# Performance work log

Measured on AMD Instinct MI355X. Metric: run time of the kernel, lower is better.

The kernel has to match this reference:

```python
import jax, jax.numpy as jnp
import numpy as np

B, P, D = 64, 196, 768
HP = WP = 14
N_CLASSES = 200
C = N_CLASSES + 1
K_PROTO = 5
GAMMA = 0.999
TEMP = 0.2
EPS_SK = 0.05
SK_ITERS = 3


def l2norm(x, axis=-1, eps=1e-12):
    n = jnp.linalg.norm(x, axis=axis, keepdims=True)
    return x / jnp.maximum(n, eps)


def _safe_div(a, b):
    return a / jnp.where(b > 0, b, 1.0)


def masked_sinkhorn(L_cnk, mask):
    """Vectorized per-class Sinkhorn-Knopp over masked patch groups.
    L_cnk: [C, N, K] logits; mask: [C, N] bool (patch n belongs to class c).
    Returns Q: [C, K, N] (columns of each present class sum to 1)."""
    m = mask[:, None, :].astype(L_cnk.dtype)  # [C,1,N]
    Q = jnp.exp(jnp.transpose(L_cnk, (0, 2, 1)) / EPS_SK) * m  # [C,K,N]
    Q = _safe_div(Q, Q.sum(axis=(1, 2), keepdims=True))
    Nc = mask.sum(axis=1).astype(Q.dtype)[:, None, None]  # per-class patch count
    Nc_safe = jnp.where(Nc > 0, Nc, 1.0)
    for _ in range(SK_ITERS):
        Q = _safe_div(Q, Q.sum(axis=2, keepdims=True)) / K_PROTO  # row (prototype) norm
        Q = _safe_div(Q, Q.sum(axis=1, keepdims=True)) / Nc_safe  # col (patch) norm
    Q = Q * Nc  # undo final /Nc -> each patch column sums to 1
    return Q


def setup_inputs() -> dict:
    key = jax.random.key(0)
    k1, k2, k3, k4, k5 = jax.random.split(key, 5)
    patch_tokens = jax.random.normal(k1, (B, P, D), dtype=jnp.float32)
    raw_patch_tokens = jax.random.normal(k2, (B, P, D), dtype=jnp.float32)
    prototypes = 0.02 * jax.random.normal(k3, (C, K_PROTO, D), dtype=jnp.float32)
    sa_weights = jnp.full((N_CLASSES, K_PROTO), 0.5, dtype=jnp.float32)
    pseudo_patch_labels = jax.random.randint(k5, (B, HP, WP), 0, C, dtype=jnp.int32)
    return {
        "patch_tokens": patch_tokens,
        "raw_patch_tokens": raw_patch_tokens,
        "prototypes": prototypes,
        "sa_weights": sa_weights,
        "pseudo_patch_labels": pseudo_patch_labels,
    }


def reference(patch_tokens, raw_patch_tokens, prototypes, sa_weights, pseudo_patch_labels):
    # --- patch-prototype cosine similarity ---
    pt = l2norm(patch_tokens)                       # [B,P,D]
    proto_n = l2norm(prototypes)                    # [C,K,D]
    logits = jnp.einsum('bpd,ckd->bpck', pt, proto_n)  # [B,P,C,K]
    image_logits = logits.max(axis=1)               # [B,C,K]
    # --- ScoreAggregation classifier ---
    sw = jax.nn.softmax(sa_weights, axis=-1) * K_PROTO  # [n_classes,K]
    class_logits = (image_logits[:, :-1, :] * sw).sum(-1) / TEMP  # [B,n_classes]
    # --- online clustering (detached in original) ---
    rpt = l2norm(raw_patch_tokens)
    patches_flat = rpt.reshape(-1, D)               # [N,D], N=B*P
    labels_flat = pseudo_patch_labels.reshape(-1)   # [N]
    N = labels_flat.shape[0]
    L_nck = logits.reshape(N, C, K_PROTO)
    L_cnk = jnp.transpose(L_nck, (1, 0, 2))         # [C,N,K]
    mask = labels_flat[None, :] == jnp.arange(C)[:, None]  # [C,N]
    Q = masked_sinkhorn(L_cnk, mask)                # [C,K,N]
    # grouped GEMM: P_c_new = Q_c @ I_c for every class at once
    P_new_c = jnp.einsum('ckn,nd->ckd', Q, patches_flat)  # [C,K,D]
    present = mask.any(axis=1)[:, None, None]
    P_new = jnp.where(present,
                      GAMMA * prototypes + (1.0 - GAMMA) * P_new_c,
                      prototypes)
    # part assignment: argmax_k Q[label_n, k, n] + label_n * K
    Q_nck = jnp.transpose(Q, (2, 0, 1))             # [N,C,K]
    Q_at = Q_nck[jnp.arange(N), labels_flat]        # [N,K]
    assign = jnp.argmax(Q_at, axis=-1).astype(jnp.int32) + labels_flat * K_PROTO
    part_assignment_maps = assign.reshape(B, HP * WP)
    return (logits, image_logits, class_logits, part_assignment_maps, P_new)
```

## Files before the change

kernel.cpp:

```cpp
#include <hip/hip_runtime.h>
#include <math.h>

#define B_ 64
#define P_ 196
#define D_ 768
#define C_ 201
#define K_ 5
#define N_ (B_*P_)
#define CK_ (C_*K_)
#define NPAD 1024
#define NCLS 200
#define GAMMA_ 0.999f
#define INV_TEMP 5.0f
#define INV_EPS 20.0f
#define CAP2 256
#define EPAD 8
#define ROWS_TOT (2*N_ + NPAD)

typedef short s16x8 __attribute__((ext_vector_type(8)));
typedef float f32x4 __attribute__((ext_vector_type(4)));
typedef unsigned short u16x4 __attribute__((ext_vector_type(4)));

typedef __attribute__((address_space(3))) void lds_void;
typedef __attribute__((address_space(1))) const void g_void;
#define GLD16(gp, lp) __builtin_amdgcn_global_load_lds((g_void*)(gp), (lds_void*)(lp), 16, 0, 0)

__device__ __forceinline__ unsigned short f2bf(float f) {
    unsigned int u = __float_as_uint(f);
    unsigned int r = (u + 0x7FFFu + ((u >> 16) & 1u)) >> 16;
    return (unsigned short)r;
}

__global__ __launch_bounds__(256) void norm_all_kernel(
        const float* __restrict__ patch, const float* __restrict__ rawp,
        const float* __restrict__ proto, float* __restrict__ invR,
        unsigned short* __restrict__ Abf, unsigned short* __restrict__ Bbf,
        int* __restrict__ cnt) {
    if (blockIdx.x == 0 && threadIdx.x < C_) cnt[threadIdx.x] = 0;
    int gw = blockIdx.x * 4 + (threadIdx.x >> 6);
    int lane = threadIdx.x & 63;
    const float* src; unsigned short* dst; int realR; int r; bool wantInv = false;
    if (gw < N_) { r = gw; src = patch; dst = Abf; realR = N_; }
    else if (gw < 2 * N_) { r = gw - N_; src = rawp; dst = nullptr; realR = N_; wantInv = true; }
    else { r = gw - 2 * N_; src = proto; dst = Bbf; realR = CK_; }
    unsigned short* brow = dst ? dst + (size_t)r * D_ : nullptr;
    if (r >= realR) {
        u16x4 z = (u16x4)0;
        *(u16x4*)(brow + lane * 4)       = z;
        *(u16x4*)(brow + lane * 4 + 256) = z;
        *(u16x4*)(brow + lane * 4 + 512) = z;
        return;
    }
    const float4* row4 = (const float4*)(src + (size_t)r * D_);
    float4 v0 = row4[lane], v1 = row4[lane + 64], v2 = row4[lane + 128];
    float s = v0.x*v0.x + v0.y*v0.y + v0.z*v0.z + v0.w*v0.w
            + v1.x*v1.x + v1.y*v1.y + v1.z*v1.z + v1.w*v1.w
            + v2.x*v2.x + v2.y*v2.y + v2.z*v2.z + v2.w*v2.w;
#pragma unroll
    for (int o = 1; o < 64; o <<= 1) s += __shfl_xor(s, o, 64);
    float sc = 1.f / fmaxf(sqrtf(s), 1e-12f);
    if (brow) {
        u16x4 p0 = { f2bf(v0.x*sc), f2bf(v0.y*sc), f2bf(v0.z*sc), f2bf(v0.w*sc) };
        u16x4 p1 = { f2bf(v1.x*sc), f2bf(v1.y*sc), f2bf(v1.z*sc), f2bf(v1.w*sc) };
        u16x4 p2 = { f2bf(v2.x*sc), f2bf(v2.y*sc), f2bf(v2.z*sc), f2bf(v2.w*sc) };
        *(u16x4*)(brow + lane * 4)       = p0;
        *(u16x4*)(brow + lane * 4 + 256) = p1;
        *(u16x4*)(brow + lane * 4 + 512) = p2;
    } else if (wantInv && lane == 0) invR[r] = sc;
}

#define BM2 256
#define BN2 256
#define BK2 64
#define KT (D_/BK2)
#define MT2 (N_/BM2)
__global__ __launch_bounds__(512, 2) void gemm_mfma_kernel(
    const unsigned short* __restrict__ Ab, const unsigned short* __restrict__ Bb,
    float* __restrict__ Cc,
    float* __restrict__ part) {
    __shared__ union {
        struct { short A[2][BM2 * BK2]; short B[2][BN2 * BK2]; } g;
        float mw[2][3][BN2];
    } u;
    int tid = threadIdx.x;
    int wid = tid >> 6;
    int lane = tid & 63;
    int wr = wid >> 2, wc = wid & 3;
    int mrow = lane & 15, q = lane >> 4;
    int slot0 = q ^ (mrow & 7);

    int orig = blockIdx.x;
    int xcd = orig & 7, idx = orig >> 3;
    int wg = (xcd < 4 ? xcd * 25 : 100 + (xcd - 4) * 24) + idx;
    int mtile = wg >> 2, ntile = wg & 3;
    int mBase = mtile * BM2;
    int nBase = ntile * BN2;

    f32x4 acc[8][4];
#pragma unroll
    for (int i = 0; i < 8; ++i)
#pragma unroll
        for (int j = 0; j < 4; ++j) acc[i][j] = (f32x4)(0.f);

    const unsigned short* gA[4];
    const unsigned short* gB[4];
    int lof[4];
#pragma unroll
    for (int s = 0; s < 4; ++s) {
        int c = tid + 512 * s;
        int row = c >> 3, ch = c & 7;
        int chx = ch ^ (row & 7);
        gA[s] = Ab + (size_t)(mBase + row) * D_ + chx * 8;
        gB[s] = Bb + (size_t)(nBase + row) * D_ + chx * 8;
        lof[s] = c * 8;
    }
    auto stage = [&](int buf, int t) {
#pragma unroll
        for (int s = 0; s < 4; ++s) GLD16(gA[s] + t * BK2, &u.g.A[buf][lof[s]]);
#pragma unroll
        for (int s = 0; s < 4; ++s) GLD16(gB[s] + t * BK2, &u.g.B[buf][lof[s]]);
    };

    stage(0, 0);
    stage(1, 1);

    for (int t = 0; t < KT; ++t) {
        int cb = t & 1;
        if (t + 1 < KT) asm volatile("s_waitcnt vmcnt(8)" ::: "memory");
        else            asm volatile("s_waitcnt vmcnt(0)" ::: "memory");
        __builtin_amdgcn_s_barrier();
        __builtin_amdgcn_sched_barrier(0);
        const short* Ac = u.g.A[cb];
        const short* Bc = u.g.B[cb];
        s16x8 a[8][2], b01[2][2], b23[2][2];
#pragma unroll
        for (int mf = 0; mf < 8; ++mf) {
            int row = wr * 128 + mf * 16 + mrow;
            a[mf][0] = *(const s16x8*)&Ac[row * 64 + slot0 * 8];
            a[mf][1] = *(const s16x8*)&Ac[row * 64 + (slot0 ^ 4) * 8];
        }
#pragma unroll
        for (int nf = 0; nf < 2; ++nf) {
            int row = wc * 64 + nf * 16 + mrow;
            b01[nf][0] = *(const s16x8*)&Bc[row * 64 + slot0 * 8];
            b01[nf][1] = *(const s16x8*)&Bc[row * 64 + (slot0 ^ 4) * 8];
        }
#pragma unroll
        for (int nf = 0; nf < 2; ++nf) {
            int row = wc * 64 + (nf + 2) * 16 + mrow;
            b23[nf][0] = *(const s16x8*)&Bc[row * 64 + slot0 * 8];
            b23[nf][1] = *(const s16x8*)&Bc[row * 64 + (slot0 ^ 4) * 8];
        }
        __builtin_amdgcn_s_setprio(1);
#pragma unroll
        for (int mf = 0; mf < 8; ++mf)
#pragma unroll
            for (int nf = 0; nf < 2; ++nf) {
                acc[mf][nf] = __builtin_amdgcn_mfma_f32_16x16x32_bf16(
                    a[mf][0], b01[nf][0], acc[mf][nf], 0, 0, 0);
                acc[mf][nf] = __builtin_amdgcn_mfma_f32_16x16x32_bf16(
                    a[mf][1], b01[nf][1], acc[mf][nf], 0, 0, 0);
            }
        __builtin_amdgcn_s_setprio(0);
        asm volatile("s_waitcnt lgkmcnt(0)" ::: "memory");
        __builtin_amdgcn_s_barrier();
        __builtin_amdgcn_sched_barrier(0);
        if (t + 2 < KT) stage(cb, t + 2);
        __builtin_amdgcn_s_setprio(1);
#pragma unroll
        for (int mf = 0; mf < 8; ++mf)
#pragma unroll
            for (int nf = 0; nf < 2; ++nf) {
                acc[mf][nf + 2] = __builtin_amdgcn_mfma_f32_16x16x32_bf16(
                    a[mf][0], b23[nf][0], acc[mf][nf + 2], 0, 0, 0);
                acc[mf][nf + 2] = __builtin_amdgcn_mfma_f32_16x16x32_bf16(
                    a[mf][1], b23[nf][1], acc[mf][nf + 2], 0, 0, 0);
            }
        __builtin_amdgcn_s_setprio(0);
    }

#pragma unroll
    for (int m = 0; m < 8; ++m) {
        int gm = mBase + wr * 128 + m * 16 + q * 4;
#pragma unroll
        for (int j = 0; j < 4; ++j) {
            int gn = nBase + wc * 64 + j * 16 + mrow;
            if (gn < CK_) {
                Cc[(size_t)(gm + 0) * CK_ + gn] = acc[m][j][0];
                Cc[(size_t)(gm + 1) * CK_ + gn] = acc[m][j][1];
                Cc[(size_t)(gm + 2) * CK_ + gn] = acc[m][j][2];
                Cc[(size_t)(gm + 3) * CK_ + gn] = acc[m][j][3];
            }
        }
    }

    int imgA = mBase / 196;
    int rs1 = 196 * (imgA + 1) - mBase;
    int rs2 = rs1 + 196;
#pragma unroll
    for (int j = 0; j < 4; ++j) {
        float m0 = -INFINITY, m1 = -INFINITY, m2 = -INFINITY;
#pragma unroll
        for (int m = 0; m < 8; ++m) {
            int lr = wr * 128 + m * 16 + q * 4;
#pragma unroll
            for (int r = 0; r < 4; ++r) {
                float v = acc[m][j][r];
                int row = lr + r;
                if (row >= rs2) m2 = fmaxf(m2, v);
                else if (row >= rs1) m1 = fmaxf(m1, v);
                else m0 = fmaxf(m0, v);
            }
        }
        m0 = fmaxf(m0, __shfl_xor(m0, 16)); m0 = fmaxf(m0, __shfl_xor(m0, 32));
        m1 = fmaxf(m1, __shfl_xor(m1, 16)); m1 = fmaxf(m1, __shfl_xor(m1, 32));
        m2 = fmaxf(m2, __shfl_xor(m2, 16)); m2 = fmaxf(m2, __shfl_xor(m2, 32));
        if (lane < 16) {
            int col = wc * 64 + j * 16 + lane;
            u.mw[wr][0][col] = m0;
            u.mw[wr][1][col] = m1;
            u.mw[wr][2][col] = m2;
        }
    }
    __syncthreads();
    if (tid < BN2) {
#pragma unroll
        for (int s = 0; s < 3; ++s) {
            float vmax = fmaxf(u.mw[0][s][tid], u.mw[1][s][tid]);
            part[(size_t)(mtile * 3 + s) * 1024 + nBase + tid] = vmax;
        }
    }
}

__global__ __launch_bounds__(256) void post_kernel(
        const float* __restrict__ part, const float* __restrict__ saw,
        float* __restrict__ img, float* __restrict__ cls,
        const float* __restrict__ L, const int* __restrict__ labels,
        int* __restrict__ cnt, int* __restrict__ idxList, float* __restrict__ EList) {
    __shared__ float simg[CK_];
    if (blockIdx.x < B_) {
        int b = blockIdx.x;
        int t0 = (196 * b) >> 8;
        int t1 = (196 * b + 195) >> 8;
        for (int n = threadIdx.x; n < CK_; n += 256) {
            float m = -INFINITY;
            for (int t = t0; t <= t1; ++t) {
                int iA = (t << 8) / 196;
                int s = b - iA;
                m = fmaxf(m, part[(size_t)(t * 3 + s) * 1024 + n]);
            }
            img[b * CK_ + n] = m;
            simg[n] = m;
        }
        __syncthreads();
        int c = threadIdx.x;
        if (c < NCLS) {
            float w[K_];
            float mx = -INFINITY;
#pragma unroll
            for (int k = 0; k < K_; ++k) { w[k] = saw[c * K_ + k]; mx = fmaxf(mx, w[k]); }
            float ssum = 0.f;
#pragma unroll
            for (int k = 0; k < K_; ++k) { w[k] = expf(w[k] - mx); ssum += w[k]; }
            float acc = 0.f;
#pragma unroll
            for (int k = 0; k < K_; ++k)
                acc += simg[c * K_ + k] * (w[k] / ssum * (float)K_);
            cls[b * NCLS + c] = acc * INV_TEMP;
        }
    } else {
        int n = (blockIdx.x - B_) * 256 + threadIdx.x;
        if (n >= N_) return;
        int c = labels[n];
        int slot = atomicAdd(&cnt[c], 1);
        if (slot < CAP2) {
            idxList[c * CAP2 + slot] = n;
            const float* lp = L + (size_t)n * CK_ + c * K_;
            float e0 = expf(lp[0] * INV_EPS), e1 = expf(lp[1] * INV_EPS);
            float e2 = expf(lp[2] * INV_EPS), e3 = expf(lp[3] * INV_EPS);
            float e4 = expf(lp[4] * INV_EPS);
            float* ep = EList + ((size_t)c * CAP2 + slot) * EPAD;
            float4 v4 = { e0, e1, e2, e3 };
            *(float4*)ep = v4;
            ep[4] = e4;
        }
    }
}

#define NJ (CAP2/64)
__global__ __launch_bounds__(768) void sinkema_kernel(
    const int* __restrict__ cnt, const int* __restrict__ idxList,
    const float* __restrict__ EList, const float* __restrict__ invR,
    const float* __restrict__ rawP, const float* __restrict__ proto,
    float* __restrict__ outAssign, float* __restrict__ outProto) {
    int c = blockIdx.x;
    int tid = threadIdx.x;
    int Nc = cnt[c]; if (Nc > CAP2) Nc = CAP2;
    size_t protoOff = (size_t)c * K_ * D_;
    if (Nc == 0) {
        for (int i = tid; i < K_ * D_; i += 768)
            outProto[protoOff + i] = proto[protoOff + i];
        return;
    }
    __shared__ float s_w[K_][CAP2];
    __shared__ int s_idx[CAP2];
    for (int i = tid; i < CAP2; i += 768)
        s_idx[i] = (i < Nc) ? idxList[c * CAP2 + i] : 0;
    __syncthreads();

    if (tid < 64) {
        int lane = tid;
        float e[NJ][K_];
        float cn[NJ];
#pragma unroll
        for (int j = 0; j < NJ; ++j) {
            int n = j * 64 + lane;
            bool v = n < Nc;
            cn[j] = v ? 1.f : 0.f;
            const float* ep = EList + ((size_t)c * CAP2 + n) * EPAD;
            float4 v4 = v ? *(const float4*)ep : make_float4(0.f, 0.f, 0.f, 0.f);
            e[j][0] = v4.x; e[j][1] = v4.y; e[j][2] = v4.z; e[j][3] = v4.w;
            e[j][4] = v ? ep[4] : 0.f;
        }
        float r[K_];
        for (int it = 0; it < 3; ++it) {
#pragma unroll
            for (int k = 0; k < K_; ++k) {
                float s = 0.f;
#pragma unroll
                for (int j = 0; j < NJ; ++j) s += e[j][k] * cn[j];
                for (int o = 32; o > 0; o >>= 1) s += __shfl_xor(s, o, 64);
                r[k] = 1.f / ((float)K_ * s);
            }
#pragma unroll
            for (int j = 0; j < NJ; ++j) {
                float t = 0.f;
#pragma unroll
                for (int k = 0; k < K_; ++k) t += e[j][k] * r[k];
                cn[j] = (j * 64 + lane < Nc) ? 1.f / ((float)Nc * t) : 0.f;
            }
        }
#pragma unroll
        for (int j = 0; j < NJ; ++j) {
            int n = j * 64 + lane;
            if (n >= Nc) continue;
            int idxn = s_idx[n];
            int kb = 0; float best = e[j][0] * r[0];
#pragma unroll
            for (int k = 1; k < K_; ++k) {
                float v = e[j][k] * r[k];
                if (v > best) { best = v; kb = k; }
            }
            outAssign[idxn] = (float)(kb + c * K_);
            float scale = cn[j] * (float)Nc * (1.0f - GAMMA_) * invR[idxn];
#pragma unroll
            for (int k = 0; k < K_; ++k)
                s_w[k][n] = e[j][k] * r[k] * scale;
        }
    }
    __syncthreads();

    float acc[K_] = {};
    int n = 0;
    for (; n + 3 < Nc; n += 4) {
        float v0 = rawP[(size_t)s_idx[n]     * D_ + tid];
        float v1 = rawP[(size_t)s_idx[n + 1] * D_ + tid];
        float v2 = rawP[(size_t)s_idx[n + 2] * D_ + tid];
        float v3 = rawP[(size_t)s_idx[n + 3] * D_ + tid];
#pragma unroll
        for (int k = 0; k < K_; ++k) {
            acc[k] = fmaf(s_w[k][n],     v0, acc[k]);
            acc[k] = fmaf(s_w[k][n + 1], v1, acc[k]);
            acc[k] = fmaf(s_w[k][n + 2], v2, acc[k]);
            acc[k] = fmaf(s_w[k][n + 3], v3, acc[k]);
        }
    }
    for (; n < Nc; ++n) {
        float v0 = rawP[(size_t)s_idx[n] * D_ + tid];
#pragma unroll
        for (int k = 0; k < K_; ++k) acc[k] = fmaf(s_w[k][n], v0, acc[k]);
    }
#pragma unroll
    for (int k = 0; k < K_; ++k) {
        size_t o = protoOff + (size_t)k * D_ + tid;
        outProto[o] = fmaf(GAMMA_, proto[o], acc[k]);
    }
}

extern "C" void kernel_launch(void* const* d_in, const int* in_sizes, int n_in,
                              void* d_out, int out_size, void* d_ws, size_t ws_size,
                              hipStream_t stream) {
    (void)in_sizes; (void)n_in; (void)out_size; (void)ws_size;
    const float* patch  = (const float*)d_in[0];
    const float* rawp   = (const float*)d_in[1];
    const float* proto  = (const float*)d_in[2];
    const float* saw    = (const float*)d_in[3];
    const int*   labels = (const int*)d_in[4];

    float* out    = (float*)d_out;
    float* logits = out;
    float* img    = out + 12606720;
    float* cls    = out + 12671040;
    float* assign = out + 12683840;
    float* pnew   = out + 12696384;

    float* ws   = (float*)d_ws;
    float* invR = ws;
    unsigned short* Abf = (unsigned short*)(ws + N_);
    unsigned short* Bbf = Abf + (size_t)N_ * D_;
    int*   cnt     = (int*)(Bbf + (size_t)NPAD * D_);
    int*   idxList = cnt + 256;
    float* EList   = (float*)(idxList + C_ * CAP2);
    float* part    = EList + (size_t)2 * C_ * K_ * CAP2;

    norm_all_kernel<<<ROWS_TOT / 4, 256, 0, stream>>>(patch, rawp, proto, invR, Abf, Bbf, cnt);
    gemm_mfma_kernel<<<MT2 * 4, 512, 0, stream>>>(Abf, Bbf, logits, part);
    post_kernel<<<B_ + N_ / 256, 256, 0, stream>>>(part, saw, img, cls, logits, labels,
                                                   cnt, idxList, EList);
    sinkema_kernel<<<C_, 768, 0, stream>>>(cnt, idxList, EList, invR, rawp, proto,
                                           assign, pnew);
}
```

Measured before the change: 179.9 us.

## Split GEMM K-step into four quadrant phases interleaving LDS reads with MFMA

Splits the main GEMM's per-K-tile work into four quadrants, A rows 0-3 and 4-7 crossed with B columns 0-1 and 2-3. Each quadrant's LDS fragment loads are followed by a barrier and its block of MFMAs. This is meant to overlap LDS reads with matrix-core work and lower peak register pressure, since only half of the A fragments are live at a time. The cost is extra workgroup barriers per iteration, which could add sync stalls. The stage of the next tile is moved later, after three of the four quadrants.

```diff
diff --git a/kernel.cpp b/kernel.cpp
--- a/kernel.cpp
+++ b/kernel.cpp
@@ -24,6 +24,7 @@
 typedef __attribute__((address_space(3))) void lds_void;
 typedef __attribute__((address_space(1))) const void g_void;
 #define GLD16(gp, lp) __builtin_amdgcn_global_load_lds((g_void*)(gp), (lds_void*)(lp), 16, 0, 0)
+#define MFMA16(a, b, c) __builtin_amdgcn_mfma_f32_16x16x32_bf16((a), (b), (c), 0, 0, 0)
 
 __device__ __forceinline__ unsigned short f2bf(float f) {
     unsigned int u = __float_as_uint(f);
@@ -132,12 +133,13 @@
         __builtin_amdgcn_sched_barrier(0);
         const short* Ac = u.g.A[cb];
         const short* Bc = u.g.B[cb];
-        s16x8 a[8][2], b01[2][2], b23[2][2];
-#pragma unroll
-        for (int mf = 0; mf < 8; ++mf) {
+        s16x8 a03[4][2], a47[4][2], b01[2][2], b23[2][2];
+
+#pragma unroll
+        for (int mf = 0; mf < 4; ++mf) {
             int row = wr * 128 + mf * 16 + mrow;
-            a[mf][0] = *(const s16x8*)&Ac[row * 64 + slot0 * 8];
-            a[mf][1] = *(const s16x8*)&Ac[row * 64 + (slot0 ^ 4) * 8];
+            a03[mf][0] = *(const s16x8*)&Ac[row * 64 + slot0 * 8];
+            a03[mf][1] = *(const s16x8*)&Ac[row * 64 + (slot0 ^ 4) * 8];
         }
 #pragma unroll
         for (int nf = 0; nf < 2; ++nf) {
@@ -145,36 +147,69 @@
             b01[nf][0] = *(const s16x8*)&Bc[row * 64 + slot0 * 8];
             b01[nf][1] = *(const s16x8*)&Bc[row * 64 + (slot0 ^ 4) * 8];
         }
+        __builtin_amdgcn_s_barrier();
+        asm volatile("s_waitcnt lgkmcnt(0)" ::: "memory");
+        __builtin_amdgcn_sched_barrier(0);
+        __builtin_amdgcn_s_setprio(1);
+#pragma unroll
+        for (int mf = 0; mf < 4; ++mf)
+#pragma unroll
+            for (int nf = 0; nf < 2; ++nf) {
+                acc[mf][nf] = MFMA16(a03[mf][0], b01[nf][0], acc[mf][nf]);
+                acc[mf][nf] = MFMA16(a03[mf][1], b01[nf][1], acc[mf][nf]);
+            }
+        __builtin_amdgcn_s_setprio(0);
+        __builtin_amdgcn_s_barrier();
+
 #pragma unroll
         for (int nf = 0; nf < 2; ++nf) {
             int row = wc * 64 + (nf + 2) * 16 + mrow;
             b23[nf][0] = *(const s16x8*)&Bc[row * 64 + slot0 * 8];
             b23[nf][1] = *(const s16x8*)&Bc[row * 64 + (slot0 ^ 4) * 8];
         }
+        __builtin_amdgcn_s_barrier();
+        asm volatile("s_waitcnt lgkmcnt(0)" ::: "memory");
+        __builtin_amdgcn_sched_barrier(0);
         __builtin_amdgcn_s_setprio(1);
 #pragma unroll
-        for (int mf = 0; mf < 8; ++mf)
+        for (int mf = 0; mf < 4; ++mf)
 #pragma unroll
             for (int nf = 0; nf < 2; ++nf) {
-                acc[mf][nf] = __builtin_amdgcn_mfma_f32_16x16x32_bf16(
-                    a[mf][0], b01[nf][0], acc[mf][nf], 0, 0, 0);
-                acc[mf][nf] = __builtin_amdgcn_mfma_f32_16x16x32_bf16(
-                    a[mf][1], b01[nf][1], acc[mf][nf], 0, 0, 0);
+                acc[mf][nf + 2] = MFMA16(a03[mf][0], b23[nf][0], acc[mf][nf + 2]);
+                acc[mf][nf + 2] = MFMA16(a03[mf][1], b23[nf][1], acc[mf][nf + 2]);
             }
         __builtin_amdgcn_s_setprio(0);
+        __builtin_amdgcn_s_barrier();
+
+#pragma unroll
+        for (int mf = 0; mf < 4; ++mf) {
+            int row = wr * 128 + (mf + 4) * 16 + mrow;
+            a47[mf][0] = *(const s16x8*)&Ac[row * 64 + slot0 * 8];
+            a47[mf][1] = *(const s16x8*)&Ac[row * 64 + (slot0 ^ 4) * 8];
+        }
+        __builtin_amdgcn_s_barrier();
         asm volatile("s_waitcnt lgkmcnt(0)" ::: "memory");
-        __builtin_amdgcn_s_barrier();
         __builtin_amdgcn_sched_barrier(0);
+        __builtin_amdgcn_s_setprio(1);
+#pragma unroll
+        for (int mf = 0; mf < 4; ++mf)
+#pragma unroll
+            for (int nf = 0; nf < 2; ++nf) {
+                acc[mf + 4][nf] = MFMA16(a47[mf][0], b01[nf][0], acc[mf + 4][nf]);
+                acc[mf + 4][nf] = MFMA16(a47[mf][1], b01[nf][1], acc[mf + 4][nf]);
+            }
+        __builtin_amdgcn_s_setprio(0);
+        __builtin_amdgcn_s_barrier();
+
         if (t + 2 < KT) stage(cb, t + 2);
+        __builtin_amdgcn_s_barrier();
         __builtin_amdgcn_s_setprio(1);
 #pragma unroll
-        for (int mf = 0; mf < 8; ++mf)
+        for (int mf = 0; mf < 4; ++mf)
 #pragma unroll
             for (int nf = 0; nf < 2; ++nf) {
-                acc[mf][nf + 2] = __builtin_amdgcn_mfma_f32_16x16x32_bf16(
-                    a[mf][0], b23[nf][0], acc[mf][nf + 2], 0, 0, 0);
-                acc[mf][nf + 2] = __builtin_amdgcn_mfma_f32_16x16x32_bf16(
-                    a[mf][1], b23[nf][1], acc[mf][nf + 2], 0, 0, 0);
+                acc[mf + 4][nf + 2] = MFMA16(a47[mf][0], b23[nf][0], acc[mf + 4][nf + 2]);
+                acc[mf + 4][nf + 2] = MFMA16(a47[mf][1], b23[nf][1], acc[mf + 4][nf + 2]);
             }
         __builtin_amdgcn_s_setprio(0);
     }
```

Measured after the change: 185.5 us. 3.1% more time.
